# Performance work log

Measured on AMD Instinct MI355X. Metric: run time of the kernel, lower is better.

Reference implementation:

```python
import jax, jax.numpy as jnp
import numpy as np

N_QUBITS = 12          # hidden_features = number of wires
QDEPTH = 8             # StronglyEntanglingLayers depth
INPUT_DIM = 784        # c*w*h = 1*28*28
DIM = 2 ** N_QUBITS    # statevector size

# bit table: wire 0 = most significant bit (PennyLane convention)
_BITS = ((np.arange(DIM)[:, None] >> np.arange(N_QUBITS - 1, -1, -1)[None, :]) & 1)  # (DIM, N)
_ZVALS = (1.0 - 2.0 * _BITS).astype(np.float32)  # (DIM, N): eigvals of PauliZ per wire

def _cz_diag(r):
    # diagonal of the product of CZ(i, (i+r)%N) for i in range(N); duplicates cancel (CZ^2=I)
    d = np.ones(DIM, np.float32)
    for i in range(N_QUBITS):
        j = (i + r) % N_QUBITS
        d *= 1.0 - 2.0 * (_BITS[:, i] * _BITS[:, j]).astype(np.float32)
    return d

# per-layer CZ entangler diagonal; PennyLane default range r = l % (N-1) + 1
_CZ_DIAGS = [jnp.asarray(_cz_diag((l % (N_QUBITS - 1)) + 1)) for l in range(QDEPTH)]


def _apply_rot(state, w3, wire):
    # Rot(phi, theta, omega) = RZ(omega) RY(theta) RZ(phi) applied to one wire
    phi, theta, omega = w3[0], w3[1], w3[2]
    c = jnp.cos(theta / 2).astype(jnp.complex64)
    s = jnp.sin(theta / 2).astype(jnp.complex64)
    m00 = jnp.exp(-0.5j * (phi + omega)) * c
    m01 = -jnp.exp(0.5j * (phi - omega)) * s
    m10 = jnp.exp(-0.5j * (phi - omega)) * s
    m11 = jnp.exp(0.5j * (phi + omega)) * c
    M = jnp.stack([jnp.stack([m00, m01]), jnp.stack([m10, m11])])  # (2,2) complex64
    b = state.shape[0]
    st = state.reshape(b, 2 ** wire, 2, -1)
    st = jnp.einsum('pq,bkqr->bkpr', M, st)
    return st.reshape(b, DIM)


def _quantum_layer(angles, qweights):
    # angles: (b, N) RZ-encoded inputs; qweights: (QDEPTH, N, 3)
    b = angles.shape[0]
    # initial |0...0>; RZ(angle_j) on |0> contributes phase exp(-i*angle_j/2)
    amp0 = jnp.exp(-0.5j * jnp.sum(angles, axis=1))  # (b,) complex64
    state = jnp.zeros((b, DIM), jnp.complex64).at[:, 0].set(amp0)
    for l in range(QDEPTH):
        for j in range(N_QUBITS):
            state = _apply_rot(state, qweights[l, j], j)
        state = state * _CZ_DIAGS[l][None, :]
    probs = state.real ** 2 + state.imag ** 2  # (b, DIM)
    return probs @ jnp.asarray(_ZVALS)         # (b, N) <Z_i> expvals


def setup_inputs() -> dict:
    key = jax.random.key(0)
    ks = jax.random.split(key, 6)
    b = 2048
    x = jax.random.normal(ks[0], (b, 1, 28, 28), jnp.float32)
    sd = 1.0 / np.sqrt(INPUT_DIM)
    su = 1.0 / np.sqrt(N_QUBITS)
    w_down = jax.random.normal(ks[1], (N_QUBITS, INPUT_DIM), jnp.float32) * sd
    b_down = jax.random.normal(ks[2], (N_QUBITS,), jnp.float32) * sd
    w_up = jax.random.normal(ks[3], (INPUT_DIM, N_QUBITS), jnp.float32) * su
    b_up = jax.random.normal(ks[4], (INPUT_DIM,), jnp.float32) * su
    qweights = jax.random.normal(ks[5], (QDEPTH, N_QUBITS, 3), jnp.float32) * 0.4
    return {"x": x, "w_down": w_down, "b_down": b_down, "w_up": w_up, "b_up": b_up, "qweights": qweights}


def reference(x, w_down, b_down, w_up, b_up, qweights):
    b, c, w, h = x.shape
    xf = x.reshape(b, -1)
    x_reduced = xf @ w_down.T + b_down            # (b, N_QUBITS)
    z = _quantum_layer(x_reduced, qweights)       # (b, N_QUBITS)
    x_restored = z @ w_up.T + b_up                # (b, INPUT_DIM)
    return x_restored.reshape(b, c, w, h)
```

## Files before the change

### kernel.cpp

```cpp
#include <hip/hip_runtime.h>

#define NQ     12
#define DIM    4096
#define QDEPTH 8
#define T      1024
#define NBLK   98

__device__ __forceinline__ int SW(int i) { return i ^ ((i >> 6) & 0xF); }

template <int KIND>
__device__ __forceinline__ float xlane(float x) {
    if constexpr (KIND == 0)
        return __int_as_float(__builtin_amdgcn_update_dpp(
            __float_as_int(x), __float_as_int(x), 0xB1, 0xF, 0xF, false));
    else if constexpr (KIND == 1)
        return __int_as_float(__builtin_amdgcn_update_dpp(
            __float_as_int(x), __float_as_int(x), 0x4E, 0xF, 0xF, false));
    else if constexpr (KIND == 2)
        return __int_as_float(__builtin_amdgcn_ds_swizzle(
            __float_as_int(x), 0x101F));
    else
        return __int_as_float(__builtin_amdgcn_update_dpp(
            __float_as_int(x), __float_as_int(x), 0x128, 0xF, 0xF, false));
}

template <int KIND>
__device__ __forceinline__ void lane_gate(float2 a[4], const float4 C) {
#pragma unroll
    for (int c = 0; c < 4; ++c) {
        const float pr = xlane<KIND>(a[c].x);
        const float pi = xlane<KIND>(a[c].y);
        const float ar = a[c].x, ai = a[c].y;
        a[c].x = C.x * ar - C.y * ai + C.z * pr - C.w * pi;
        a[c].y = C.x * ai + C.y * ar + C.z * pi + C.w * pr;
    }
}

__device__ __forceinline__ void reg_gate(float2 a[4], const int m,
                                         const float4 V0, const float4 V1) {
#pragma unroll
    for (int c = 0; c < 4; ++c) {
        if (c & m) continue;
        const int c1 = c | m;
        const float a0r = a[c].x,  a0i = a[c].y;
        const float a1r = a[c1].x, a1i = a[c1].y;
        a[c].x  = V0.x * a0r - V0.y * a0i + V0.z * a1r - V0.w * a1i;
        a[c].y  = V0.x * a0i + V0.y * a0r + V0.z * a1i + V0.w * a1r;
        a[c1].x = V1.z * a0r - V1.w * a0i + V1.x * a1r - V1.y * a1i;
        a[c1].y = V1.z * a0i + V1.w * a0r + V1.x * a1i + V1.y * a1r;
    }
}

__device__ __forceinline__ void load_coefs(const float4* __restrict__ m2,
                                           const int gi0, const int lane,
                                           float4 R[8]) {
    const float4* G = m2 + gi0 * 2;
    R[0] = G[0]; R[1] = G[1]; R[2] = G[2]; R[3] = G[3];
    R[4] = G[4  + ((lane >> 3) & 1)];
    R[5] = G[6  + ((lane >> 2) & 1)];
    R[6] = G[8  + ((lane >> 1) & 1)];
    R[7] = G[10 + ( lane       & 1)];
}

__device__ __forceinline__ void apply6(float2 a[4], const float4 R[8]) {
    reg_gate(a, 2, R[0], R[1]);
    reg_gate(a, 1, R[2], R[3]);
    lane_gate<3>(a, R[4]);
    lane_gate<2>(a, R[5]);
    lane_gate<1>(a, R[6]);
    lane_gate<0>(a, R[7]);
}

__device__ __forceinline__ void apply_cz(float2 a[4], const int ii[4], const int d) {
    const int r = d + 1;
#pragma unroll
    for (int c = 0; c < 4; ++c) {
        const unsigned i  = (unsigned)ii[c];
        const unsigned ro = ((i << r) | (i >> (12 - r))) & 0xFFFu;
        if (__popc(i & ro) & 1) { a[c].x = -a[c].x; a[c].y = -a[c].y; }
    }
}

__device__ __forceinline__ void merged_pass(float2* __restrict__ st,
                                            const float4* __restrict__ m2,
                                            const int ja[4], const int ii[4],
                                            const int gbase, const int l1,
                                            const int d, const int lane,
                                            float2 a[4]) {
    float4 R1[8], R2[8];
    load_coefs(m2, l1 * NQ + gbase, lane, R1);
    __syncthreads();
#pragma unroll
    for (int c = 0; c < 4; ++c) a[c] = st[ja[c]];
    load_coefs(m2, (d + 1) * NQ + gbase, lane, R2);
    apply6(a, R1);
    apply_cz(a, ii, d);
    apply6(a, R2);
#pragma unroll
    for (int c = 0; c < 4; ++c) st[ja[c]] = a[c];
}

__global__ __launch_bounds__(T) void qnn_fused(const float* __restrict__ qw,
                                               const float* __restrict__ w_up,
                                               const float* __restrict__ b_up,
                                               float* __restrict__ out) {
    __shared__ float2 st[DIM];
    __shared__ float4 mats2[96 * 2];
    __shared__ float  zred[T / 64][NQ];
    __shared__ float  zfin[NQ];
    __shared__ float4 row4[196];

    const int tid  = threadIdx.x;
    const int lane = tid & 63;

    if (tid < 96) {
        const float phi = qw[tid * 3 + 0], theta = qw[tid * 3 + 1], omega = qw[tid * 3 + 2];
        float c, s, sp, cp, sm, cm;
        sincosf(0.5f * theta, &s, &c);
        sincosf(0.5f * (phi + omega), &sp, &cp);
        sincosf(0.5f * (phi - omega), &sm, &cm);
        mats2[tid * 2 + 0] = make_float4(cp * c, -sp * c, -cm * s, -sm * s);
        mats2[tid * 2 + 1] = make_float4(cp * c,  sp * c,  cm * s, -sm * s);
    }
    __syncthreads();

    const int w4 = (tid >> 6) & 0xF, l54 = (tid >> 4) & 3, l30 = tid & 0xF;
    int jaA[4], iiA[4], jaB[4], iiB[4];
#pragma unroll
    for (int c = 0; c < 4; ++c) {
        iiA[c] = (c << 10) | (l30 << 6) | (l54 << 4) | w4;
        iiB[c] = (l54 << 10) | (w4 << 6) | (c << 4) | l30;
        jaA[c] = SW(iiA[c]);
        jaB[c] = SW(iiB[c]);
    }

    float2 a[4];
    {
        float4 R1[8], R2[8];
        load_coefs(mats2, 0 * NQ + 6, lane, R1);
        load_coefs(mats2, 1 * NQ + 6, lane, R2);
        const int h = (l54 << 4) | w4;
        float pr = 1.f, pi = 0.f;
#pragma unroll
        for (int k = 0; k < 6; ++k) {
            const int b = (h >> (5 - k)) & 1;
            const float4 g0 = mats2[2 * k], g1 = mats2[2 * k + 1];
            const float cr = b ? g1.z : g0.x;
            const float ci = b ? g1.w : g0.y;
            const float nr = pr * cr - pi * ci;
            const float ni = pr * ci + pi * cr;
            pr = nr; pi = ni;
        }
        a[0] = (l30 == 0) ? make_float2(pr, pi) : make_float2(0.f, 0.f);
        a[1] = a[2] = a[3] = make_float2(0.f, 0.f);
        apply6(a, R1);
        apply_cz(a, iiB, 0);
        apply6(a, R2);
#pragma unroll
        for (int c = 0; c < 4; ++c) st[jaB[c]] = a[c];
    }
    merged_pass(st, mats2, jaA, iiA, 0, 1, 1, lane, a);
    merged_pass(st, mats2, jaB, iiB, 6, 2, 2, lane, a);
    merged_pass(st, mats2, jaA, iiA, 0, 3, 3, lane, a);
    merged_pass(st, mats2, jaB, iiB, 6, 4, 4, lane, a);
    merged_pass(st, mats2, jaA, iiA, 0, 5, 5, lane, a);
    merged_pass(st, mats2, jaB, iiB, 6, 6, 6, lane, a);
    {
        float4 R1[8];
        load_coefs(mats2, 7 * NQ + 0, lane, R1);
        __syncthreads();
#pragma unroll
        for (int c = 0; c < 4; ++c) a[c] = st[jaA[c]];
        apply6(a, R1);
    }

    float zp[NQ];
#pragma unroll
    for (int w = 0; w < NQ; ++w) zp[w] = 0.0f;
#pragma unroll
    for (int c = 0; c < 4; ++c) {
        const float pr = a[c].x * a[c].x + a[c].y * a[c].y;
        const int i = iiA[c];
#pragma unroll
        for (int w = 0; w < NQ; ++w) zp[w] += ((i >> (11 - w)) & 1) ? -pr : pr;
    }
#pragma unroll
    for (int w = 0; w < NQ; ++w) {
        float v = zp[w];
        for (int off = 32; off > 0; off >>= 1) v += __shfl_down(v, off, 64);
        zp[w] = v;
    }
    const int wave = tid >> 6;
    if (lane == 0) {
#pragma unroll
        for (int w = 0; w < NQ; ++w) zred[wave][w] = zp[w];
    }
    __syncthreads();
    if (tid < NQ) {
        float v = 0.0f;
#pragma unroll
        for (int k = 0; k < T / 64; ++k) v += zred[k][tid];
        zfin[tid] = v;
    }
    __syncthreads();

    if (tid < 784) {
        float acc = b_up[tid];
#pragma unroll
        for (int j = 0; j < NQ; ++j) acc += zfin[j] * w_up[tid * NQ + j];
        ((float*)row4)[tid] = acc;
    }
    __syncthreads();

    const int idx = blockIdx.x * T + tid;
    const float4 v = row4[idx % 196];
    float4* o = (float4*)out;
#pragma unroll
    for (int k = 0; k < 4; ++k) o[idx + k * 100352] = v;
}

extern "C" void kernel_launch(void* const* d_in, const int* in_sizes, int n_in,
                              void* d_out, int out_size, void* d_ws, size_t ws_size,
                              hipStream_t stream) {
    const float* w_up = (const float*)d_in[3];
    const float* b_up = (const float*)d_in[4];
    const float* qw   = (const float*)d_in[5];
    float* out = (float*)d_out;

    qnn_fused<<<NBLK, T, 0, stream>>>(qw, w_up, b_up, out);
}
```

Measured before the change: 90.30 us.

## Spread output writes over 256 blocks, pack complex math, and streamline the Z reduction

The grid grows from 98 to 256 blocks, and each block now writes eight contiguous output rows instead of a strided slice. The goal is to spread the store traffic across all CUs, at the cost of each block still running the full redundant statevector simulation. Complex gate arithmetic is rewritten on 2-wide ext_vector floats so the compiler can emit packed FP32 ops. The per-wire Z expectation drops the per-bit loop by using the known index structure. The wave reduction uses DPP and swizzle steps plus readlane instead of shuffle-down, and coefficient setup now uses 192 threads instead of 96.

```diff
diff --git a/kernel.cpp b/kernel.cpp
--- a/kernel.cpp
+++ b/kernel.cpp
@@ -4,50 +4,53 @@
 #define DIM    4096
 #define QDEPTH 8
 #define T      1024
-#define NBLK   98
+#define NBLK   256
+
+typedef float v2f __attribute__((ext_vector_type(2)));
 
 __device__ __forceinline__ int SW(int i) { return i ^ ((i >> 6) & 0xF); }
+
+template <int CTRL>
+__device__ __forceinline__ float dpp_mov(float x) {
+    return __int_as_float(__builtin_amdgcn_update_dpp(
+        __float_as_int(x), __float_as_int(x), CTRL, 0xF, 0xF, false));
+}
+
+__device__ __forceinline__ float swz_xor4(float x) {
+    return __int_as_float(__builtin_amdgcn_ds_swizzle(
+        __float_as_int(x), 0x101F));
+}
 
 template <int KIND>
 __device__ __forceinline__ float xlane(float x) {
-    if constexpr (KIND == 0)
-        return __int_as_float(__builtin_amdgcn_update_dpp(
-            __float_as_int(x), __float_as_int(x), 0xB1, 0xF, 0xF, false));
-    else if constexpr (KIND == 1)
-        return __int_as_float(__builtin_amdgcn_update_dpp(
-            __float_as_int(x), __float_as_int(x), 0x4E, 0xF, 0xF, false));
-    else if constexpr (KIND == 2)
-        return __int_as_float(__builtin_amdgcn_ds_swizzle(
-            __float_as_int(x), 0x101F));
-    else
-        return __int_as_float(__builtin_amdgcn_update_dpp(
-            __float_as_int(x), __float_as_int(x), 0x128, 0xF, 0xF, false));
-}
+    if constexpr (KIND == 0) return dpp_mov<0xB1>(x);
+    else if constexpr (KIND == 1) return dpp_mov<0x4E>(x);
+    else if constexpr (KIND == 2) return swz_xor4(x);
+    else return dpp_mov<0x128>(x);
+}
+
+__device__ __forceinline__ v2f jmul(const v2f a) { return (v2f){ -a.y, a.x }; }
 
 template <int KIND>
-__device__ __forceinline__ void lane_gate(float2 a[4], const float4 C) {
-#pragma unroll
-    for (int c = 0; c < 4; ++c) {
-        const float pr = xlane<KIND>(a[c].x);
-        const float pi = xlane<KIND>(a[c].y);
-        const float ar = a[c].x, ai = a[c].y;
-        a[c].x = C.x * ar - C.y * ai + C.z * pr - C.w * pi;
-        a[c].y = C.x * ai + C.y * ar + C.z * pi + C.w * pr;
-    }
-}
-
-__device__ __forceinline__ void reg_gate(float2 a[4], const int m,
+__device__ __forceinline__ void lane_gate(v2f a[4], const float4 C) {
+#pragma unroll
+    for (int c = 0; c < 4; ++c) {
+        const v2f own = a[c];
+        const v2f p = (v2f){ xlane<KIND>(own.x), xlane<KIND>(own.y) };
+        a[c] = C.x * own + C.y * jmul(own) + C.z * p + C.w * jmul(p);
+    }
+}
+
+__device__ __forceinline__ void reg_gate(v2f a[4], const int m,
                                          const float4 V0, const float4 V1) {
 #pragma unroll
     for (int c = 0; c < 4; ++c) {
         if (c & m) continue;
         const int c1 = c | m;
-        const float a0r = a[c].x,  a0i = a[c].y;
-        const float a1r = a[c1].x, a1i = a[c1].y;
-        a[c].x  = V0.x * a0r - V0.y * a0i + V0.z * a1r - V0.w * a1i;
-        a[c].y  = V0.x * a0i + V0.y * a0r + V0.z * a1i + V0.w * a1r;
-        a[c1].x = V1.z * a0r - V1.w * a0i + V1.x * a1r - V1.y * a1i;
-        a[c1].y = V1.z * a0i + V1.w * a0r + V1.x * a1i + V1.y * a1r;
+        const v2f a0 = a[c], a1 = a[c1];
+        const v2f j0 = jmul(a0), j1 = jmul(a1);
+        a[c]  = V0.x * a0 + V0.y * j0 + V0.z * a1 + V0.w * j1;
+        a[c1] = V1.z * a0 + V1.w * j0 + V1.x * a1 + V1.y * j1;
     }
 }
 
@@ -62,7 +65,7 @@
     R[7] = G[10 + ( lane       & 1)];
 }
 
-__device__ __forceinline__ void apply6(float2 a[4], const float4 R[8]) {
+__device__ __forceinline__ void apply6(v2f a[4], const float4 R[8]) {
     reg_gate(a, 2, R[0], R[1]);
     reg_gate(a, 1, R[2], R[3]);
     lane_gate<3>(a, R[4]);
@@ -71,30 +74,30 @@
     lane_gate<0>(a, R[7]);
 }
 
-__device__ __forceinline__ void apply_cz(float2 a[4], const int ii[4], const int d) {
+__device__ __forceinline__ void apply_cz(v2f a[4], const int ii[4], const int d) {
     const int r = d + 1;
 #pragma unroll
     for (int c = 0; c < 4; ++c) {
         const unsigned i  = (unsigned)ii[c];
         const unsigned ro = ((i << r) | (i >> (12 - r))) & 0xFFFu;
-        if (__popc(i & ro) & 1) { a[c].x = -a[c].x; a[c].y = -a[c].y; }
-    }
-}
-
-__device__ __forceinline__ void merged_pass(float2* __restrict__ st,
+        const float s = (__popc(i & ro) & 1) ? -1.f : 1.f;
+        a[c] *= s;
+    }
+}
+
+__device__ __forceinline__ void merged_pass(v2f* __restrict__ st,
                                             const float4* __restrict__ m2,
                                             const int ja[4], const int ii[4],
                                             const int gbase, const int l1,
-                                            const int d, const int lane,
-                                            float2 a[4]) {
+                                            const int lane, v2f a[4]) {
     float4 R1[8], R2[8];
     load_coefs(m2, l1 * NQ + gbase, lane, R1);
     __syncthreads();
 #pragma unroll
     for (int c = 0; c < 4; ++c) a[c] = st[ja[c]];
-    load_coefs(m2, (d + 1) * NQ + gbase, lane, R2);
+    load_coefs(m2, (l1 + 1) * NQ + gbase, lane, R2);
     apply6(a, R1);
-    apply_cz(a, ii, d);
+    apply_cz(a, ii, l1);
     apply6(a, R2);
 #pragma unroll
     for (int c = 0; c < 4; ++c) st[ja[c]] = a[c];
@@ -104,7 +107,7 @@
                                                const float* __restrict__ w_up,
                                                const float* __restrict__ b_up,
                                                float* __restrict__ out) {
-    __shared__ float2 st[DIM];
+    __shared__ v2f    st[DIM];
     __shared__ float4 mats2[96 * 2];
     __shared__ float  zred[T / 64][NQ];
     __shared__ float  zfin[NQ];
@@ -113,14 +116,15 @@
     const int tid  = threadIdx.x;
     const int lane = tid & 63;
 
-    if (tid < 96) {
-        const float phi = qw[tid * 3 + 0], theta = qw[tid * 3 + 1], omega = qw[tid * 3 + 2];
+    if (tid < 192) {
+        const int g = tid >> 1, h = tid & 1;
+        const float phi = qw[g * 3 + 0], theta = qw[g * 3 + 1], omega = qw[g * 3 + 2];
         float c, s, sp, cp, sm, cm;
         sincosf(0.5f * theta, &s, &c);
         sincosf(0.5f * (phi + omega), &sp, &cp);
         sincosf(0.5f * (phi - omega), &sm, &cm);
-        mats2[tid * 2 + 0] = make_float4(cp * c, -sp * c, -cm * s, -sm * s);
-        mats2[tid * 2 + 1] = make_float4(cp * c,  sp * c,  cm * s, -sm * s);
+        mats2[g * 2 + h] = h ? make_float4(cp * c,  sp * c,  cm * s, -sm * s)
+                             : make_float4(cp * c, -sp * c, -cm * s, -sm * s);
     }
     __syncthreads();
 
@@ -134,37 +138,35 @@
         jaB[c] = SW(iiB[c]);
     }
 
-    float2 a[4];
+    v2f a[4];
     {
         float4 R1[8], R2[8];
         load_coefs(mats2, 0 * NQ + 6, lane, R1);
         load_coefs(mats2, 1 * NQ + 6, lane, R2);
         const int h = (l54 << 4) | w4;
-        float pr = 1.f, pi = 0.f;
+        v2f p = (v2f){ 1.f, 0.f };
 #pragma unroll
         for (int k = 0; k < 6; ++k) {
             const int b = (h >> (5 - k)) & 1;
             const float4 g0 = mats2[2 * k], g1 = mats2[2 * k + 1];
             const float cr = b ? g1.z : g0.x;
             const float ci = b ? g1.w : g0.y;
-            const float nr = pr * cr - pi * ci;
-            const float ni = pr * ci + pi * cr;
-            pr = nr; pi = ni;
+            p = cr * p + ci * jmul(p);
         }
-        a[0] = (l30 == 0) ? make_float2(pr, pi) : make_float2(0.f, 0.f);
-        a[1] = a[2] = a[3] = make_float2(0.f, 0.f);
+        a[0] = (l30 == 0) ? p : (v2f){ 0.f, 0.f };
+        a[1] = a[2] = a[3] = (v2f){ 0.f, 0.f };
         apply6(a, R1);
         apply_cz(a, iiB, 0);
         apply6(a, R2);
 #pragma unroll
         for (int c = 0; c < 4; ++c) st[jaB[c]] = a[c];
     }
-    merged_pass(st, mats2, jaA, iiA, 0, 1, 1, lane, a);
-    merged_pass(st, mats2, jaB, iiB, 6, 2, 2, lane, a);
-    merged_pass(st, mats2, jaA, iiA, 0, 3, 3, lane, a);
-    merged_pass(st, mats2, jaB, iiB, 6, 4, 4, lane, a);
-    merged_pass(st, mats2, jaA, iiA, 0, 5, 5, lane, a);
-    merged_pass(st, mats2, jaB, iiB, 6, 6, 6, lane, a);
+    merged_pass(st, mats2, jaA, iiA, 0, 1, lane, a);
+    merged_pass(st, mats2, jaB, iiB, 6, 2, lane, a);
+    merged_pass(st, mats2, jaA, iiA, 0, 3, lane, a);
+    merged_pass(st, mats2, jaB, iiB, 6, 4, lane, a);
+    merged_pass(st, mats2, jaA, iiA, 0, 5, lane, a);
+    merged_pass(st, mats2, jaB, iiB, 6, 6, lane, a);
     {
         float4 R1[8];
         load_coefs(mats2, 7 * NQ + 0, lane, R1);
@@ -174,21 +176,30 @@
         apply6(a, R1);
     }
 
+    float p4[4];
+#pragma unroll
+    for (int c = 0; c < 4; ++c) p4[c] = a[c].x * a[c].x + a[c].y * a[c].y;
+    const float s01 = p4[0] + p4[1], s23 = p4[2] + p4[3];
+    const float S = s01 + s23;
     float zp[NQ];
-#pragma unroll
-    for (int w = 0; w < NQ; ++w) zp[w] = 0.0f;
-#pragma unroll
-    for (int c = 0; c < 4; ++c) {
-        const float pr = a[c].x * a[c].x + a[c].y * a[c].y;
-        const int i = iiA[c];
-#pragma unroll
-        for (int w = 0; w < NQ; ++w) zp[w] += ((i >> (11 - w)) & 1) ? -pr : pr;
-    }
+    zp[0] = s01 - s23;
+    zp[1] = (p4[0] - p4[1]) + (p4[2] - p4[3]);
+#pragma unroll
+    for (int w = 2; w < NQ; ++w)
+        zp[w] = (((iiA[0] >> (11 - w)) & 1) ? -S : S);
+
 #pragma unroll
     for (int w = 0; w < NQ; ++w) {
         float v = zp[w];
-        for (int off = 32; off > 0; off >>= 1) v += __shfl_down(v, off, 64);
-        zp[w] = v;
+        v += dpp_mov<0xB1>(v);
+        v += dpp_mov<0x4E>(v);
+        v += swz_xor4(v);
+        v += dpp_mov<0x128>(v);
+        const float r0 = __int_as_float(__builtin_amdgcn_readlane(__float_as_int(v), 0));
+        const float r1 = __int_as_float(__builtin_amdgcn_readlane(__float_as_int(v), 16));
+        const float r2 = __int_as_float(__builtin_amdgcn_readlane(__float_as_int(v), 32));
+        const float r3 = __int_as_float(__builtin_amdgcn_readlane(__float_as_int(v), 48));
+        zp[w] = (r0 + r1) + (r2 + r3);
     }
     const int wave = tid >> 6;
     if (lane == 0) {
@@ -212,11 +223,13 @@
     }
     __syncthreads();
 
-    const int idx = blockIdx.x * T + tid;
-    const float4 v = row4[idx % 196];
-    float4* o = (float4*)out;
-#pragma unroll
-    for (int k = 0; k < 4; ++k) o[idx + k * 100352] = v;
+    if (tid < 784) {
+        const float4 v = row4[tid % 196];
+        float4* o = (float4*)out;
+        const int base = blockIdx.x * 1568;
+        o[base + tid]       = v;
+        o[base + 784 + tid] = v;
+    }
 }
 
 extern "C" void kernel_launch(void* const* d_in, const int* in_sizes, int n_in,
```

New measurement: 97.00 us. 1.07x slower.
